# Kernel optimization log

Measured on AMD Instinct MI355X. Metric: run time of the kernel, lower is better.

Reference implementation:

```python
import jax, jax.numpy as jnp
import numpy as np

B = 65536
H = 1024          # hidden_dimension
D_OUT = 2         # output_dimension
N_EXPERTS = 10


def setup_inputs() -> dict:
    key = jax.random.key(0)
    ks = jax.random.split(key, 9)
    s = 0.02
    return {
        "x": jax.random.normal(ks[0], (B, 12), dtype=jnp.float32),
        "W1": jax.random.normal(ks[1], (H, 1), dtype=jnp.float32) * s,    # fc1 weight [out,in]
        "b1": jax.random.normal(ks[2], (H,), dtype=jnp.float32) * s,
        "Wmeta": jax.random.normal(ks[3], (N_EXPERTS, H), dtype=jnp.float32) * s,  # row i = fc_meta[i].weight[:,0]
        "bmeta": jax.random.normal(ks[4], (N_EXPERTS, H), dtype=jnp.float32) * s,  # row i = fc_meta[i].bias
        "W2": jax.random.normal(ks[5], (H, H), dtype=jnp.float32) * s,
        "b2": jax.random.normal(ks[6], (H,), dtype=jnp.float32) * s,
        "W3": jax.random.normal(ks[7], (D_OUT, H), dtype=jnp.float32) * s,
        "b3": jax.random.normal(ks[8], (D_OUT,), dtype=jnp.float32) * s,
    }


def reference(x, W1, b1, Wmeta, bmeta, W2, b2, W3, b3):
    one_hot = x[:, 0:10]          # [B, 10] expert selection weights
    delta = x[:, 10:11]           # [B, 1]
    phi = x[:, 11:12]             # [B, 1]
    # fc1(delta): [B,1] @ [1,H]
    x1 = delta * W1[:, 0] + b1    # [B, H]
    # expert i output: phi * Wmeta[i] + bmeta[i]; one-hot weighted sum over experts
    # sum_i one_hot[:,i]*(phi*Wmeta[i]+bmeta[i]) = phi*(one_hot@Wmeta) + one_hot@bmeta
    x2 = phi * (one_hot @ Wmeta) + one_hot @ bmeta  # [B, H]
    h = jax.nn.relu(x1 + x2)
    h = jax.nn.relu(h @ W2.T + b2)                  # fc2 + relu
    return h @ W3.T + b3                            # fc3 -> [B, 2]
```

## Files before the change

kernel.cpp:

```cpp
#include <hip/hip_runtime.h>
#include <stdint.h>

#define NROWS 65536
#define HD 1024

typedef __attribute__((ext_vector_type(8))) short bf16x8;
typedef __attribute__((ext_vector_type(16))) float f32x16;

typedef __attribute__((address_space(1))) const unsigned int* gas_ptr;
typedef __attribute__((address_space(3))) unsigned int* las_ptr;

__device__ __forceinline__ unsigned short f2bf(float f) {
  union { float f; uint32_t u; } v; v.f = f;
  uint32_t u = v.u;
  return (unsigned short)((u + 0x7fffu + ((u >> 16) & 1u)) >> 16);
}

__device__ __forceinline__ void gl16(const void* g, void* l) {
  __builtin_amdgcn_global_load_lds((gas_ptr)g, (las_ptr)l, 16, 0, 0);
}

__global__ void k_w2pk(const float* __restrict__ W2, unsigned short* __restrict__ W2pk) {
  int i = blockIdx.x * 256 + threadIdx.x;
  int lane = i & 63, f = (i >> 6) & 15, T = (i >> 10) & 15, ct = i >> 14;
  int kl = f & 1, p = (f >> 1) & 1, cb = (f >> 2) & 1, wn = f >> 3;
  int col = ct * 128 + wn * 64 + cb * 32 + (lane & 31);
  int k = T * 64 + p * 32 + kl * 16 + (lane >> 5) * 8;
  const float4* s4 = (const float4*)(W2 + (size_t)col * HD + k);
  float4 a = s4[0], b = s4[1];
  uint4 pk;
  pk.x = (uint32_t)f2bf(a.x) | ((uint32_t)f2bf(a.y) << 16);
  pk.y = (uint32_t)f2bf(a.z) | ((uint32_t)f2bf(a.w) << 16);
  pk.z = (uint32_t)f2bf(b.x) | ((uint32_t)f2bf(b.y) << 16);
  pk.w = (uint32_t)f2bf(b.z) | ((uint32_t)f2bf(b.w) << 16);
  *(uint4*)(W2pk + (size_t)i * 8) = pk;
}

__global__ __launch_bounds__(512) void k_layer1(
    const float* __restrict__ x, const float* __restrict__ W1,
    const float* __restrict__ b1, const float* __restrict__ Wmeta,
    const float* __restrict__ bmeta, unsigned short* __restrict__ h) {
  __shared__ float xs[64 * 12];
  int r0 = blockIdx.x * 64;
  int t = threadIdx.x;
  int j0 = t * 2;
  float w1a = W1[j0], w1b = W1[j0 + 1];
  float b1a = b1[j0], b1b = b1[j0 + 1];
  float wma[10], wmb[10], bma[10], bmb[10];
#pragma unroll
  for (int e = 0; e < 10; e++) {
    float2 wmv = *(const float2*)(Wmeta + e * HD + j0);
    float2 bmv = *(const float2*)(bmeta + e * HD + j0);
    wma[e] = wmv.x; wmb[e] = wmv.y; bma[e] = bmv.x; bmb[e] = bmv.y;
  }
  for (int i = t; i < 64 * 12; i += 512) xs[i] = x[(size_t)r0 * 12 + i];
  __syncthreads();
  int g = j0 >> 3;
  for (int r = 0; r < 64; r++) {
    const float* xr = xs + r * 12;
    float delta = xr[10], phi = xr[11];
    float s1a = 0.f, s1b = 0.f, s2a = 0.f, s2b = 0.f;
#pragma unroll
    for (int e = 0; e < 10; e++) {
      float oh = xr[e];
      s1a = fmaf(oh, wma[e], s1a);
      s1b = fmaf(oh, wmb[e], s1b);
      s2a = fmaf(oh, bma[e], s2a);
      s2b = fmaf(oh, bmb[e], s2b);
    }
    float pa = fmaf(delta, w1a, b1a) + fmaf(phi, s1a, s2a);
    float pb = fmaf(delta, w1b, b1b) + fmaf(phi, s1b, s2b);
    pa = fmaxf(pa, 0.f); pb = fmaxf(pb, 0.f);
    uint32_t pk = (uint32_t)f2bf(pa) | ((uint32_t)f2bf(pb) << 16);
    int rr = r0 + r;
    int gs = (g & 124) | ((g & 3) ^ ((rr >> 1) & 3));
    *(uint32_t*)(h + (size_t)rr * HD + gs * 8 + (j0 & 7)) = pk;
  }
}

__global__ __launch_bounds__(256, 4) void k_gemm(
    const unsigned short* __restrict__ h, const unsigned short* __restrict__ W2pk,
    const float* __restrict__ b2, const float* __restrict__ W3,
    float* __restrict__ partial) {
  __shared__ char lds[34816];
  int tid = threadIdx.x;
  int b = (int)blockIdx.x;
  int bx = ((b & 7) << 9) | (b >> 3);
  int rt = bx >> 3, ct = bx & 7;
  size_t r0 = (size_t)rt * 128;
  int c0 = ct * 128;
  int w = tid >> 6, lane = tid & 63;
  int wm = w >> 1, wn = w & 1;
  int l31 = lane & 31, hi = lane >> 5;
  int sw = (l31 >> 1) & 3;

  f32x16 acc[2][2];
#pragma unroll
  for (int rb = 0; rb < 2; rb++)
#pragma unroll
    for (int cb = 0; cb < 2; cb++)
#pragma unroll
      for (int i = 0; i < 16; i++) acc[rb][cb][i] = 0.f;

  int arow0 = (wm * 64 + 0  + l31) * 64;
  int arow1 = (wm * 64 + 32 + l31) * 64;
  const unsigned short* bwave = W2pk + ((size_t)ct * 16 * 16 + (size_t)wn * 8) * 512 + lane * 8;

  for (int T = 0; T < 16; T++) {
    const unsigned short* bt = bwave + (size_t)T * 16 * 512;
    bf16x8 B[2][4];
#pragma unroll
    for (int cb = 0; cb < 2; cb++)
#pragma unroll
      for (int pk = 0; pk < 4; pk++)
        B[cb][pk] = *(const bf16x8*)(bt + (cb * 4 + pk) * 512);
#pragma unroll
    for (int q = 0; q < 2; q++) {
      int s = tid + 256 * q;
      int row = s >> 2, g4 = s & 3;
      const unsigned short* hsrc = h + (r0 + row) * (size_t)HD + T * 64 + g4 * 8;
      gl16(hsrc,      lds +        (size_t)s * 16);
      gl16(hsrc + 32, lds + 8192 + (size_t)s * 16);
    }
    __syncthreads();
#pragma unroll
    for (int p = 0; p < 2; p++) {
      const char* lA = lds + p * 8192;
#pragma unroll
      for (int kl = 0; kl < 2; kl++) {
        int slot = ((kl * 2 + hi) ^ sw) << 4;
        bf16x8 a0 = *(const bf16x8*)(lA + arow0 + slot);
        bf16x8 a1 = *(const bf16x8*)(lA + arow1 + slot);
        acc[0][0] = __builtin_amdgcn_mfma_f32_32x32x16_bf16(a0, B[0][p * 2 + kl], acc[0][0], 0, 0, 0);
        acc[0][1] = __builtin_amdgcn_mfma_f32_32x32x16_bf16(a0, B[1][p * 2 + kl], acc[0][1], 0, 0, 0);
        acc[1][0] = __builtin_amdgcn_mfma_f32_32x32x16_bf16(a1, B[0][p * 2 + kl], acc[1][0], 0, 0, 0);
        acc[1][1] = __builtin_amdgcn_mfma_f32_32x32x16_bf16(a1, B[1][p * 2 + kl], acc[1][1], 0, 0, 0);
      }
    }
    __syncthreads();
  }

  float b2c[2], w30[2], w31[2];
#pragma unroll
  for (int cb = 0; cb < 2; cb++) {
    int c = c0 + wn * 64 + cb * 32 + l31;
    b2c[cb] = b2[c];
    w30[cb] = W3[c];
    w31[cb] = W3[HD + c];
  }
  float2* sE = (float2*)lds;
#pragma unroll
  for (int rb = 0; rb < 2; rb++) {
    __syncthreads();
#pragma unroll
    for (int reg = 0; reg < 16; reg++) {
      float v0 = fmaxf(acc[rb][0][reg] + b2c[0], 0.f);
      float v1 = fmaxf(acc[rb][1][reg] + b2c[1], 0.f);
      float2 o;
      o.x = v0 * w30[0] + v1 * w30[1];
      o.y = v0 * w31[0] + v1 * w31[1];
      int rowf = (reg & 3) + 8 * (reg >> 2) + 4 * hi;
      int line = (wm * 32 + rowf) * 2 + wn;
      sE[line * 33 + l31] = o;
    }
    __syncthreads();
    int half = tid & 1, tgt = tid >> 1;
    int d = tgt & 1, rowf_t = (tgt >> 1) & 31, bi = tgt >> 6;
    int line0 = (bi * 32 + rowf_t) * 2 + half;
    const float* sf = (const float*)lds;
    float s = 0.f;
#pragma unroll
    for (int j = 0; j < 32; j++) s += sf[(line0 * 33 + j) * 2 + d];
    s += __shfl_xor(s, 1);
    if (half == 0) {
      int row = bi * 64 + rb * 32 + rowf_t;
      partial[(size_t)ct * (NROWS * 2) + (r0 + row) * 2 + d] = s;
    }
  }
}

__global__ void k_reduce(const float* __restrict__ partial, const float* __restrict__ b3,
                         float* __restrict__ out) {
  int i = blockIdx.x * 256 + threadIdx.x;
  float s = b3[i & 1];
#pragma unroll
  for (int ctt = 0; ctt < 8; ctt++) s += partial[(size_t)ctt * 131072 + i];
  out[i] = s;
}

extern "C" void kernel_launch(void* const* d_in, const int* in_sizes, int n_in,
                              void* d_out, int out_size, void* d_ws, size_t ws_size,
                              hipStream_t stream) {
  const float* x     = (const float*)d_in[0];
  const float* W1    = (const float*)d_in[1];
  const float* b1    = (const float*)d_in[2];
  const float* Wmeta = (const float*)d_in[3];
  const float* bmeta = (const float*)d_in[4];
  const float* W2    = (const float*)d_in[5];
  const float* b2    = (const float*)d_in[6];
  const float* W3    = (const float*)d_in[7];
  const float* b3    = (const float*)d_in[8];
  float* out = (float*)d_out;

  char* ws = (char*)d_ws;
  unsigned short* hbuf  = (unsigned short*)ws;
  unsigned short* W2pk  = (unsigned short*)(ws + (size_t)NROWS * HD * 2);
  float* partial = (float*)(ws + (size_t)NROWS * HD * 2 + (size_t)HD * HD * 2);

  k_w2pk<<<512, 256, 0, stream>>>(W2, W2pk);
  k_layer1<<<1024, 512, 0, stream>>>(x, W1, b1, Wmeta, bmeta, hbuf);
  k_gemm<<<4096, 256, 0, stream>>>(hbuf, W2pk, b2, W3, partial);
  k_reduce<<<512, 256, 0, stream>>>(partial, b3, out);
}
```

Measured before the change: 204.6 us.

## Restructure fc2 GEMM into per-wave 64x64 tiles with double-buffered A/B prefetch

```diff
diff --git a/kernel.cpp b/kernel.cpp
--- a/kernel.cpp
+++ b/kernel.cpp
@@ -22,9 +22,9 @@
 
 __global__ void k_w2pk(const float* __restrict__ W2, unsigned short* __restrict__ W2pk) {
   int i = blockIdx.x * 256 + threadIdx.x;
-  int lane = i & 63, f = (i >> 6) & 15, T = (i >> 10) & 15, ct = i >> 14;
-  int kl = f & 1, p = (f >> 1) & 1, cb = (f >> 2) & 1, wn = f >> 3;
-  int col = ct * 128 + wn * 64 + cb * 32 + (lane & 31);
+  int lane = i & 63, f = (i >> 6) & 7, T = (i >> 9) & 15, ct = i >> 13;
+  int kl = f & 1, p = (f >> 1) & 1, cb = f >> 2;
+  int col = ct * 64 + cb * 32 + (lane & 31);
   int k = T * 64 + p * 32 + kl * 16 + (lane >> 5) * 8;
   const float4* s4 = (const float4*)(W2 + (size_t)col * HD + k);
   float4 a = s4[0], b = s4[1];
@@ -73,26 +73,25 @@
     pa = fmaxf(pa, 0.f); pb = fmaxf(pb, 0.f);
     uint32_t pk = (uint32_t)f2bf(pa) | ((uint32_t)f2bf(pb) << 16);
     int rr = r0 + r;
-    int gs = (g & 124) | ((g & 3) ^ ((rr >> 1) & 3));
+    int gs = (g & 120) | ((g & 7) ^ (rr & 7));
     *(uint32_t*)(h + (size_t)rr * HD + gs * 8 + (j0 & 7)) = pk;
   }
 }
 
-__global__ __launch_bounds__(256, 4) void k_gemm(
+__global__ __launch_bounds__(256, 2) void k_gemm(
     const unsigned short* __restrict__ h, const unsigned short* __restrict__ W2pk,
     const float* __restrict__ b2, const float* __restrict__ W3,
     float* __restrict__ partial) {
-  __shared__ char lds[34816];
+  __shared__ char lds[65536];
   int tid = threadIdx.x;
   int b = (int)blockIdx.x;
   int bx = ((b & 7) << 9) | (b >> 3);
-  int rt = bx >> 3, ct = bx & 7;
-  size_t r0 = (size_t)rt * 128;
-  int c0 = ct * 128;
+  int rblk = bx >> 4, ct = bx & 15;
+  size_t r0 = (size_t)rblk * 256;
+  int c0 = ct * 64;
   int w = tid >> 6, lane = tid & 63;
-  int wm = w >> 1, wn = w & 1;
   int l31 = lane & 31, hi = lane >> 5;
-  int sw = (l31 >> 1) & 3;
+  char* ldsw = lds + w * 16384;
 
   f32x16 acc[2][2];
 #pragma unroll
@@ -102,79 +101,81 @@
 #pragma unroll
       for (int i = 0; i < 16; i++) acc[rb][cb][i] = 0.f;
 
-  int arow0 = (wm * 64 + 0  + l31) * 64;
-  int arow1 = (wm * 64 + 32 + l31) * 64;
-  const unsigned short* bwave = W2pk + ((size_t)ct * 16 * 16 + (size_t)wn * 8) * 512 + lane * 8;
-
+  const unsigned short* aSrc = h + (r0 + w * 64 + (lane >> 3)) * (size_t)HD + (lane & 7) * 8;
+  const unsigned short* bSrc = W2pk + ((size_t)ct * 8192 + lane) * 8;
+
+#define STAGE_A(T, BUF)                                                           \
+  do {                                                                            \
+    _Pragma("unroll")                                                             \
+    for (int q = 0; q < 8; q++)                                                   \
+      gl16(aSrc + (size_t)q * 8 * HD + (T) * 64,                                  \
+           ldsw + (BUF) * 8192 + q * 1024 + (lane & 63) * 16);                    \
+  } while (0)
+
+  bf16x8 B[2][8];
+  STAGE_A(0, 0);
+#pragma unroll
+  for (int f = 0; f < 8; f++) B[0][f] = *(const bf16x8*)(bSrc + (0 * 512 + f * 64) * 8);
+
+  int slotBase = l31 & 7;
+#pragma unroll
   for (int T = 0; T < 16; T++) {
-    const unsigned short* bt = bwave + (size_t)T * 16 * 512;
-    bf16x8 B[2][4];
-#pragma unroll
-    for (int cb = 0; cb < 2; cb++)
-#pragma unroll
-      for (int pk = 0; pk < 4; pk++)
-        B[cb][pk] = *(const bf16x8*)(bt + (cb * 4 + pk) * 512);
-#pragma unroll
-    for (int q = 0; q < 2; q++) {
-      int s = tid + 256 * q;
-      int row = s >> 2, g4 = s & 3;
-      const unsigned short* hsrc = h + (r0 + row) * (size_t)HD + T * 64 + g4 * 8;
-      gl16(hsrc,      lds +        (size_t)s * 16);
-      gl16(hsrc + 32, lds + 8192 + (size_t)s * 16);
-    }
-    __syncthreads();
-#pragma unroll
-    for (int p = 0; p < 2; p++) {
-      const char* lA = lds + p * 8192;
-#pragma unroll
-      for (int kl = 0; kl < 2; kl++) {
-        int slot = ((kl * 2 + hi) ^ sw) << 4;
-        bf16x8 a0 = *(const bf16x8*)(lA + arow0 + slot);
-        bf16x8 a1 = *(const bf16x8*)(lA + arow1 + slot);
-        acc[0][0] = __builtin_amdgcn_mfma_f32_32x32x16_bf16(a0, B[0][p * 2 + kl], acc[0][0], 0, 0, 0);
-        acc[0][1] = __builtin_amdgcn_mfma_f32_32x32x16_bf16(a0, B[1][p * 2 + kl], acc[0][1], 0, 0, 0);
-        acc[1][0] = __builtin_amdgcn_mfma_f32_32x32x16_bf16(a1, B[0][p * 2 + kl], acc[1][0], 0, 0, 0);
-        acc[1][1] = __builtin_amdgcn_mfma_f32_32x32x16_bf16(a1, B[1][p * 2 + kl], acc[1][1], 0, 0, 0);
-      }
-    }
-    __syncthreads();
+    const int cur = T & 1, nxt = cur ^ 1;
+    if (T < 15) {
+      STAGE_A(T + 1, nxt);
+#pragma unroll
+      for (int f = 0; f < 8; f++)
+        B[nxt][f] = *(const bf16x8*)(bSrc + ((T + 1) * 512 + f * 64) * 8);
+    }
+    if (T < 15) { asm volatile("s_waitcnt vmcnt(16)" ::: "memory"); }
+    else        { asm volatile("s_waitcnt vmcnt(0)" ::: "memory"); }
+    __builtin_amdgcn_sched_barrier(0);
+    bf16x8 a0[4], a1[4];
+#pragma unroll
+    for (int s = 0; s < 4; s++) {
+      int sl = ((s * 2 + hi) ^ slotBase) << 4;
+      a0[s] = *(const bf16x8*)(ldsw + cur * 8192 + l31 * 128 + sl);
+      a1[s] = *(const bf16x8*)(ldsw + cur * 8192 + (l31 + 32) * 128 + sl);
+    }
+    asm volatile("s_waitcnt lgkmcnt(0)" ::: "memory");
+    __builtin_amdgcn_sched_barrier(0);
+    __builtin_amdgcn_s_setprio(1);
+#pragma unroll
+    for (int s = 0; s < 4; s++) {
+      acc[0][0] = __builtin_amdgcn_mfma_f32_32x32x16_bf16(a0[s], B[cur][s],     acc[0][0], 0, 0, 0);
+      acc[0][1] = __builtin_amdgcn_mfma_f32_32x32x16_bf16(a0[s], B[cur][4 + s], acc[0][1], 0, 0, 0);
+      acc[1][0] = __builtin_amdgcn_mfma_f32_32x32x16_bf16(a1[s], B[cur][s],     acc[1][0], 0, 0, 0);
+      acc[1][1] = __builtin_amdgcn_mfma_f32_32x32x16_bf16(a1[s], B[cur][4 + s], acc[1][1], 0, 0, 0);
+    }
+    __builtin_amdgcn_s_setprio(0);
   }
 
   float b2c[2], w30[2], w31[2];
 #pragma unroll
   for (int cb = 0; cb < 2; cb++) {
-    int c = c0 + wn * 64 + cb * 32 + l31;
+    int c = c0 + cb * 32 + l31;
     b2c[cb] = b2[c];
     w30[cb] = W3[c];
     w31[cb] = W3[HD + c];
   }
-  float2* sE = (float2*)lds;
 #pragma unroll
   for (int rb = 0; rb < 2; rb++) {
-    __syncthreads();
 #pragma unroll
     for (int reg = 0; reg < 16; reg++) {
       float v0 = fmaxf(acc[rb][0][reg] + b2c[0], 0.f);
       float v1 = fmaxf(acc[rb][1][reg] + b2c[1], 0.f);
-      float2 o;
-      o.x = v0 * w30[0] + v1 * w30[1];
-      o.y = v0 * w31[0] + v1 * w31[1];
-      int rowf = (reg & 3) + 8 * (reg >> 2) + 4 * hi;
-      int line = (wm * 32 + rowf) * 2 + wn;
-      sE[line * 33 + l31] = o;
-    }
-    __syncthreads();
-    int half = tid & 1, tgt = tid >> 1;
-    int d = tgt & 1, rowf_t = (tgt >> 1) & 31, bi = tgt >> 6;
-    int line0 = (bi * 32 + rowf_t) * 2 + half;
-    const float* sf = (const float*)lds;
-    float s = 0.f;
-#pragma unroll
-    for (int j = 0; j < 32; j++) s += sf[(line0 * 33 + j) * 2 + d];
-    s += __shfl_xor(s, 1);
-    if (half == 0) {
-      int row = bi * 64 + rb * 32 + rowf_t;
-      partial[(size_t)ct * (NROWS * 2) + (r0 + row) * 2 + d] = s;
+      float o0 = fmaf(v0, w30[0], v1 * w30[1]);
+      float o1 = fmaf(v0, w31[0], v1 * w31[1]);
+#pragma unroll
+      for (int m = 16; m >= 1; m >>= 1) {
+        o0 += __shfl_xor(o0, m);
+        o1 += __shfl_xor(o1, m);
+      }
+      if (l31 == 0) {
+        size_t row = r0 + w * 64 + rb * 32 + (reg & 3) + 8 * (reg >> 2) + 4 * hi;
+        float2 o; o.x = o0; o.y = o1;
+        *(float2*)(partial + (size_t)ct * (NROWS * 2) + row * 2) = o;
+      }
     }
   }
 }
@@ -184,7 +185,7 @@
   int i = blockIdx.x * 256 + threadIdx.x;
   float s = b3[i & 1];
 #pragma unroll
-  for (int ctt = 0; ctt < 8; ctt++) s += partial[(size_t)ctt * 131072 + i];
+  for (int ctt = 0; ctt < 16; ctt++) s += partial[(size_t)ctt * 131072 + i];
   out[i] = s;
 }
 
```

New measurement: 267.5 us. +30.7%, slower.

## Triple-buffer A tiles and double-buffer B fragments in GEMM; merge prep kernels

Applied to the files above, without the earlier changes.

```diff
diff --git a/kernel.cpp b/kernel.cpp
--- a/kernel.cpp
+++ b/kernel.cpp
@@ -20,28 +20,29 @@
   __builtin_amdgcn_global_load_lds((gas_ptr)g, (las_ptr)l, 16, 0, 0);
 }
 
-__global__ void k_w2pk(const float* __restrict__ W2, unsigned short* __restrict__ W2pk) {
-  int i = blockIdx.x * 256 + threadIdx.x;
-  int lane = i & 63, f = (i >> 6) & 15, T = (i >> 10) & 15, ct = i >> 14;
-  int kl = f & 1, p = (f >> 1) & 1, cb = (f >> 2) & 1, wn = f >> 3;
-  int col = ct * 128 + wn * 64 + cb * 32 + (lane & 31);
-  int k = T * 64 + p * 32 + kl * 16 + (lane >> 5) * 8;
-  const float4* s4 = (const float4*)(W2 + (size_t)col * HD + k);
-  float4 a = s4[0], b = s4[1];
-  uint4 pk;
-  pk.x = (uint32_t)f2bf(a.x) | ((uint32_t)f2bf(a.y) << 16);
-  pk.y = (uint32_t)f2bf(a.z) | ((uint32_t)f2bf(a.w) << 16);
-  pk.z = (uint32_t)f2bf(b.x) | ((uint32_t)f2bf(b.y) << 16);
-  pk.w = (uint32_t)f2bf(b.z) | ((uint32_t)f2bf(b.w) << 16);
-  *(uint4*)(W2pk + (size_t)i * 8) = pk;
-}
-
-__global__ __launch_bounds__(512) void k_layer1(
+__global__ __launch_bounds__(512) void k_prep(
     const float* __restrict__ x, const float* __restrict__ W1,
     const float* __restrict__ b1, const float* __restrict__ Wmeta,
-    const float* __restrict__ bmeta, unsigned short* __restrict__ h) {
+    const float* __restrict__ bmeta, const float* __restrict__ W2,
+    unsigned short* __restrict__ h, unsigned short* __restrict__ W2pk) {
   __shared__ float xs[64 * 12];
-  int r0 = blockIdx.x * 64;
+  if (blockIdx.x < 256) {
+    int i = blockIdx.x * 512 + threadIdx.x;
+    int lane = i & 63, f = (i >> 6) & 15, T = (i >> 10) & 15, ct = i >> 14;
+    int kl = f & 1, p = (f >> 1) & 1, cb = (f >> 2) & 1, wn = f >> 3;
+    int col = ct * 128 + wn * 64 + cb * 32 + (lane & 31);
+    int k = T * 64 + p * 32 + kl * 16 + (lane >> 5) * 8;
+    const float4* s4 = (const float4*)(W2 + (size_t)col * HD + k);
+    float4 a = s4[0], b = s4[1];
+    uint4 pk;
+    pk.x = (uint32_t)f2bf(a.x) | ((uint32_t)f2bf(a.y) << 16);
+    pk.y = (uint32_t)f2bf(a.z) | ((uint32_t)f2bf(a.w) << 16);
+    pk.z = (uint32_t)f2bf(b.x) | ((uint32_t)f2bf(b.y) << 16);
+    pk.w = (uint32_t)f2bf(b.z) | ((uint32_t)f2bf(b.w) << 16);
+    *(uint4*)(W2pk + (size_t)i * 8) = pk;
+    return;
+  }
+  int r0 = ((int)blockIdx.x - 256) * 64;
   int t = threadIdx.x;
   int j0 = t * 2;
   float w1a = W1[j0], w1b = W1[j0 + 1];
@@ -78,11 +79,11 @@
   }
 }
 
-__global__ __launch_bounds__(256, 4) void k_gemm(
+__global__ __launch_bounds__(256, 3) void k_gemm(
     const unsigned short* __restrict__ h, const unsigned short* __restrict__ W2pk,
     const float* __restrict__ b2, const float* __restrict__ W3,
     float* __restrict__ partial) {
-  __shared__ char lds[34816];
+  __shared__ char lds[49152];
   int tid = threadIdx.x;
   int b = (int)blockIdx.x;
   int bx = ((b & 7) << 9) | (b >> 3);
@@ -93,6 +94,8 @@
   int wm = w >> 1, wn = w & 1;
   int l31 = lane & 31, hi = lane >> 5;
   int sw = (l31 >> 1) & 3;
+  int s0 = (hi ^ sw) << 4;
+  int s1 = ((2 + hi) ^ sw) << 4;
 
   f32x16 acc[2][2];
 #pragma unroll
@@ -104,41 +107,93 @@
 
   int arow0 = (wm * 64 + 0  + l31) * 64;
   int arow1 = (wm * 64 + 32 + l31) * 64;
-  const unsigned short* bwave = W2pk + ((size_t)ct * 16 * 16 + (size_t)wn * 8) * 512 + lane * 8;
-
-  for (int T = 0; T < 16; T++) {
-    const unsigned short* bt = bwave + (size_t)T * 16 * 512;
-    bf16x8 B[2][4];
-#pragma unroll
-    for (int cb = 0; cb < 2; cb++)
-#pragma unroll
-      for (int pk = 0; pk < 4; pk++)
-        B[cb][pk] = *(const bf16x8*)(bt + (cb * 4 + pk) * 512);
-#pragma unroll
-    for (int q = 0; q < 2; q++) {
-      int s = tid + 256 * q;
-      int row = s >> 2, g4 = s & 3;
-      const unsigned short* hsrc = h + (r0 + row) * (size_t)HD + T * 64 + g4 * 8;
-      gl16(hsrc,      lds +        (size_t)s * 16);
-      gl16(hsrc + 32, lds + 8192 + (size_t)s * 16);
-    }
-    __syncthreads();
-#pragma unroll
-    for (int p = 0; p < 2; p++) {
-      const char* lA = lds + p * 8192;
-#pragma unroll
-      for (int kl = 0; kl < 2; kl++) {
-        int slot = ((kl * 2 + hi) ^ sw) << 4;
-        bf16x8 a0 = *(const bf16x8*)(lA + arow0 + slot);
-        bf16x8 a1 = *(const bf16x8*)(lA + arow1 + slot);
-        acc[0][0] = __builtin_amdgcn_mfma_f32_32x32x16_bf16(a0, B[0][p * 2 + kl], acc[0][0], 0, 0, 0);
-        acc[0][1] = __builtin_amdgcn_mfma_f32_32x32x16_bf16(a0, B[1][p * 2 + kl], acc[0][1], 0, 0, 0);
-        acc[1][0] = __builtin_amdgcn_mfma_f32_32x32x16_bf16(a1, B[0][p * 2 + kl], acc[1][0], 0, 0, 0);
-        acc[1][1] = __builtin_amdgcn_mfma_f32_32x32x16_bf16(a1, B[1][p * 2 + kl], acc[1][1], 0, 0, 0);
-      }
-    }
-    __syncthreads();
-  }
+  const unsigned short* bwave = W2pk + ((size_t)ct * 256 + (size_t)wn * 8) * 512 + lane * 8;
+
+#define STAGE_A(T, SB)                                                            \
+  do {                                                                            \
+    _Pragma("unroll")                                                             \
+    for (int q = 0; q < 2; q++) {                                                 \
+      int s = tid + 256 * q;                                                      \
+      int row = s >> 2, g4 = s & 3;                                               \
+      const unsigned short* hsrc = h + (r0 + row) * (size_t)HD + (T) * 64 + g4 * 8; \
+      gl16(hsrc,      lds + (SB) +        (size_t)s * 16);                        \
+      gl16(hsrc + 32, lds + (SB) + 8192 + (size_t)s * 16);                        \
+    }                                                                             \
+  } while (0)
+
+#define GBODY(T, BC, BN)                                                          \
+  do {                                                                            \
+    const char* lA0 = lds + slotT;                                                \
+    const char* lA1 = lds + slotT + 8192;                                         \
+    bf16x8 a00 = *(const bf16x8*)(lA0 + arow0 + s0);              \
+    bf16x8 a01 = *(const bf16x8*)(lA0 + arow1 + s0);                              \
+    bf16x8 a02 = *(const bf16x8*)(lA0 + arow0 + s1);                  \
+    bf16x8 a03 = *(const bf16x8*)(lA0 + arow1 + s1);                              \
+    bf16x8 a10 = *(const bf16x8*)(lA1 + arow0 + s0);                  \
+    bf16x8 a11 = *(const bf16x8*)(lA1 + arow1 + s0);                              \
+    bf16x8 a12 = *(const bf16x8*)(lA1 + arow0 + s1);                  \
+    bf16x8 a13 = *(const bf16x8*)(lA1 + arow1 + s1);                              \
+    if ((T) < 14) STAGE_A((T) + 2, slotS);                                        \
+    const unsigned short* btn = bwave + (size_t)((T) + 1) * 8192;                 \
+    if ((T) < 15) {                                                               \
+      BN[0] = *(const bf16x8*)(btn + 0 * 512);                                    \
+      BN[1] = *(const bf16x8*)(btn + 1 * 512);                                    \
+      BN[2] = *(const bf16x8*)(btn + 2 * 512);                                    \
+      BN[3] = *(const bf16x8*)(btn + 3 * 512);                                    \
+    }                                                                             \
+    if ((T) <= 13)      { asm volatile("s_waitcnt vmcnt(8)" ::: "memory"); }      \
+    else if ((T) == 14) { asm volatile("s_waitcnt vmcnt(4)" ::: "memory"); }      \
+    else                { asm volatile("s_waitcnt vmcnt(0)" ::: "memory"); }      \
+    asm volatile("s_waitcnt lgkmcnt(0)" ::: "memory");                            \
+    __builtin_amdgcn_sched_barrier(0);                                            \
+    __builtin_amdgcn_s_setprio(1);                                                \
+    acc[0][0] = __builtin_amdgcn_mfma_f32_32x32x16_bf16(a00, BC[0], acc[0][0], 0, 0, 0); \
+    acc[1][0] = __builtin_amdgcn_mfma_f32_32x32x16_bf16(a01, BC[0], acc[1][0], 0, 0, 0); \
+    acc[0][0] = __builtin_amdgcn_mfma_f32_32x32x16_bf16(a02, BC[1], acc[0][0], 0, 0, 0); \
+    acc[1][0] = __builtin_amdgcn_mfma_f32_32x32x16_bf16(a03, BC[1], acc[1][0], 0, 0, 0); \
+    acc[0][0] = __builtin_amdgcn_mfma_f32_32x32x16_bf16(a10, BC[2], acc[0][0], 0, 0, 0); \
+    acc[1][0] = __builtin_amdgcn_mfma_f32_32x32x16_bf16(a11, BC[2], acc[1][0], 0, 0, 0); \
+    acc[0][0] = __builtin_amdgcn_mfma_f32_32x32x16_bf16(a12, BC[3], acc[0][0], 0, 0, 0); \
+    acc[1][0] = __builtin_amdgcn_mfma_f32_32x32x16_bf16(a13, BC[3], acc[1][0], 0, 0, 0); \
+    __builtin_amdgcn_s_setprio(0);                                                \
+    if ((T) < 15) {                                                               \
+      BN[4] = *(const bf16x8*)(btn + 4 * 512);                                    \
+      BN[5] = *(const bf16x8*)(btn + 5 * 512);                                    \
+      BN[6] = *(const bf16x8*)(btn + 6 * 512);                                    \
+      BN[7] = *(const bf16x8*)(btn + 7 * 512);                                    \
+    }                                                                             \
+    __builtin_amdgcn_s_setprio(1);                                                \
+    acc[0][1] = __builtin_amdgcn_mfma_f32_32x32x16_bf16(a00, BC[4], acc[0][1], 0, 0, 0); \
+    acc[1][1] = __builtin_amdgcn_mfma_f32_32x32x16_bf16(a01, BC[4], acc[1][1], 0, 0, 0); \
+    acc[0][1] = __builtin_amdgcn_mfma_f32_32x32x16_bf16(a02, BC[5], acc[0][1], 0, 0, 0); \
+    acc[1][1] = __builtin_amdgcn_mfma_f32_32x32x16_bf16(a03, BC[5], acc[1][1], 0, 0, 0); \
+    acc[0][1] = __builtin_amdgcn_mfma_f32_32x32x16_bf16(a10, BC[6], acc[0][1], 0, 0, 0); \
+    acc[1][1] = __builtin_amdgcn_mfma_f32_32x32x16_bf16(a11, BC[6], acc[1][1], 0, 0, 0); \
+    acc[0][1] = __builtin_amdgcn_mfma_f32_32x32x16_bf16(a12, BC[7], acc[0][1], 0, 0, 0); \
+    acc[1][1] = __builtin_amdgcn_mfma_f32_32x32x16_bf16(a13, BC[7], acc[1][1], 0, 0, 0); \
+    __builtin_amdgcn_s_setprio(0);                                                \
+    __builtin_amdgcn_s_barrier();                                                 \
+    slotT += 16384; if (slotT == 49152) slotT = 0;                                \
+    slotS += 16384; if (slotS == 49152) slotS = 0;                                \
+  } while (0)
+
+  bf16x8 B0s[8], B1s[8];
+  {
+    const unsigned short* bt0 = bwave;
+#pragma unroll
+    for (int f = 0; f < 8; f++) B0s[f] = *(const bf16x8*)(bt0 + f * 512);
+  }
+  STAGE_A(0, 0);
+  STAGE_A(1, 16384);
+  asm volatile("s_waitcnt vmcnt(4)" ::: "memory");
+  __builtin_amdgcn_s_barrier();
+
+  int slotT = 0, slotS = 32768;
+  for (int TT = 0; TT < 8; TT++) {
+    GBODY(TT * 2,     B0s, B1s);
+    GBODY(TT * 2 + 1, B1s, B0s);
+  }
+  __syncthreads();
 
   float b2c[2], w30[2], w31[2];
 #pragma unroll
@@ -207,8 +262,7 @@
   unsigned short* W2pk  = (unsigned short*)(ws + (size_t)NROWS * HD * 2);
   float* partial = (float*)(ws + (size_t)NROWS * HD * 2 + (size_t)HD * HD * 2);
 
-  k_w2pk<<<512, 256, 0, stream>>>(W2, W2pk);
-  k_layer1<<<1024, 512, 0, stream>>>(x, W1, b1, Wmeta, bmeta, hbuf);
+  k_prep<<<1280, 512, 0, stream>>>(x, W1, b1, Wmeta, bmeta, W2, hbuf, W2pk);
   k_gemm<<<4096, 256, 0, stream>>>(hbuf, W2pk, b2, W3, partial);
   k_reduce<<<512, 256, 0, stream>>>(partial, b3, out);
 }
```

New measurement: 214.5 us. 1.05x slower.

## Fuse prep kernels and replace partial-sum reduce with shuffle reduction plus atomics

Applied to the files above, without the earlier changes.

```diff
diff --git a/kernel.cpp b/kernel.cpp
--- a/kernel.cpp
+++ b/kernel.cpp
@@ -20,28 +20,31 @@
   __builtin_amdgcn_global_load_lds((gas_ptr)g, (las_ptr)l, 16, 0, 0);
 }
 
-__global__ void k_w2pk(const float* __restrict__ W2, unsigned short* __restrict__ W2pk) {
-  int i = blockIdx.x * 256 + threadIdx.x;
-  int lane = i & 63, f = (i >> 6) & 15, T = (i >> 10) & 15, ct = i >> 14;
-  int kl = f & 1, p = (f >> 1) & 1, cb = (f >> 2) & 1, wn = f >> 3;
-  int col = ct * 128 + wn * 64 + cb * 32 + (lane & 31);
-  int k = T * 64 + p * 32 + kl * 16 + (lane >> 5) * 8;
-  const float4* s4 = (const float4*)(W2 + (size_t)col * HD + k);
-  float4 a = s4[0], b = s4[1];
-  uint4 pk;
-  pk.x = (uint32_t)f2bf(a.x) | ((uint32_t)f2bf(a.y) << 16);
-  pk.y = (uint32_t)f2bf(a.z) | ((uint32_t)f2bf(a.w) << 16);
-  pk.z = (uint32_t)f2bf(b.x) | ((uint32_t)f2bf(b.y) << 16);
-  pk.w = (uint32_t)f2bf(b.z) | ((uint32_t)f2bf(b.w) << 16);
-  *(uint4*)(W2pk + (size_t)i * 8) = pk;
-}
-
-__global__ __launch_bounds__(512) void k_layer1(
+__global__ __launch_bounds__(512) void k_prep(
     const float* __restrict__ x, const float* __restrict__ W1,
     const float* __restrict__ b1, const float* __restrict__ Wmeta,
-    const float* __restrict__ bmeta, unsigned short* __restrict__ h) {
+    const float* __restrict__ bmeta, const float* __restrict__ W2,
+    const float* __restrict__ b3, unsigned short* __restrict__ h,
+    unsigned short* __restrict__ W2pk, float* __restrict__ out) {
   __shared__ float xs[64 * 12];
-  int r0 = blockIdx.x * 64;
+  if (blockIdx.x < 256) {
+    int i = blockIdx.x * 512 + threadIdx.x;
+    out[i] = b3[i & 1];
+    int lane = i & 63, f = (i >> 6) & 15, T = (i >> 10) & 15, ct = i >> 14;
+    int kl = f & 1, p = (f >> 1) & 1, cb = (f >> 2) & 1, wn = f >> 3;
+    int col = ct * 128 + wn * 64 + cb * 32 + (lane & 31);
+    int k = T * 64 + p * 32 + kl * 16 + (lane >> 5) * 8;
+    const float4* s4 = (const float4*)(W2 + (size_t)col * HD + k);
+    float4 a = s4[0], b = s4[1];
+    uint4 pk;
+    pk.x = (uint32_t)f2bf(a.x) | ((uint32_t)f2bf(a.y) << 16);
+    pk.y = (uint32_t)f2bf(a.z) | ((uint32_t)f2bf(a.w) << 16);
+    pk.z = (uint32_t)f2bf(b.x) | ((uint32_t)f2bf(b.y) << 16);
+    pk.w = (uint32_t)f2bf(b.z) | ((uint32_t)f2bf(b.w) << 16);
+    *(uint4*)(W2pk + (size_t)i * 8) = pk;
+    return;
+  }
+  int r0 = ((int)blockIdx.x - 256) * 64;
   int t = threadIdx.x;
   int j0 = t * 2;
   float w1a = W1[j0], w1b = W1[j0 + 1];
@@ -81,8 +84,8 @@
 __global__ __launch_bounds__(256, 4) void k_gemm(
     const unsigned short* __restrict__ h, const unsigned short* __restrict__ W2pk,
     const float* __restrict__ b2, const float* __restrict__ W3,
-    float* __restrict__ partial) {
-  __shared__ char lds[34816];
+    float* __restrict__ out) {
+  __shared__ char lds[16384];
   int tid = threadIdx.x;
   int b = (int)blockIdx.x;
   int bx = ((b & 7) << 9) | (b >> 3);
@@ -148,44 +151,26 @@
     w30[cb] = W3[c];
     w31[cb] = W3[HD + c];
   }
-  float2* sE = (float2*)lds;
 #pragma unroll
   for (int rb = 0; rb < 2; rb++) {
-    __syncthreads();
 #pragma unroll
     for (int reg = 0; reg < 16; reg++) {
       float v0 = fmaxf(acc[rb][0][reg] + b2c[0], 0.f);
       float v1 = fmaxf(acc[rb][1][reg] + b2c[1], 0.f);
-      float2 o;
-      o.x = v0 * w30[0] + v1 * w30[1];
-      o.y = v0 * w31[0] + v1 * w31[1];
-      int rowf = (reg & 3) + 8 * (reg >> 2) + 4 * hi;
-      int line = (wm * 32 + rowf) * 2 + wn;
-      sE[line * 33 + l31] = o;
-    }
-    __syncthreads();
-    int half = tid & 1, tgt = tid >> 1;
-    int d = tgt & 1, rowf_t = (tgt >> 1) & 31, bi = tgt >> 6;
-    int line0 = (bi * 32 + rowf_t) * 2 + half;
-    const float* sf = (const float*)lds;
-    float s = 0.f;
+      float o0 = fmaf(v0, w30[0], v1 * w30[1]);
+      float o1 = fmaf(v0, w31[0], v1 * w31[1]);
 #pragma unroll
-    for (int j = 0; j < 32; j++) s += sf[(line0 * 33 + j) * 2 + d];
-    s += __shfl_xor(s, 1);
-    if (half == 0) {
-      int row = bi * 64 + rb * 32 + rowf_t;
-      partial[(size_t)ct * (NROWS * 2) + (r0 + row) * 2 + d] = s;
+      for (int m = 1; m <= 16; m <<= 1) {
+        o0 += __shfl_xor(o0, m);
+        o1 += __shfl_xor(o1, m);
+      }
+      if (l31 == 0) {
+        size_t row = r0 + wm * 64 + rb * 32 + (reg & 3) + 8 * (reg >> 2) + 4 * hi;
+        atomicAdd(&out[row * 2 + 0], o0);
+        atomicAdd(&out[row * 2 + 1], o1);
+      }
     }
   }
-}
-
-__global__ void k_reduce(const float* __restrict__ partial, const float* __restrict__ b3,
-                         float* __restrict__ out) {
-  int i = blockIdx.x * 256 + threadIdx.x;
-  float s = b3[i & 1];
-#pragma unroll
-  for (int ctt = 0; ctt < 8; ctt++) s += partial[(size_t)ctt * 131072 + i];
-  out[i] = s;
 }
 
 extern "C" void kernel_launch(void* const* d_in, const int* in_sizes, int n_in,
@@ -205,10 +190,7 @@
   char* ws = (char*)d_ws;
   unsigned short* hbuf  = (unsigned short*)ws;
   unsigned short* W2pk  = (unsigned short*)(ws + (size_t)NROWS * HD * 2);
-  float* partial = (float*)(ws + (size_t)NROWS * HD * 2 + (size_t)HD * HD * 2);
 
-  k_w2pk<<<512, 256, 0, stream>>>(W2, W2pk);
-  k_layer1<<<1024, 512, 0, stream>>>(x, W1, b1, Wmeta, bmeta, hbuf);
-  k_gemm<<<4096, 256, 0, stream>>>(hbuf, W2pk, b2, W3, partial);
-  k_reduce<<<512, 256, 0, stream>>>(partial, b3, out);
+  k_prep<<<1280, 512, 0, stream>>>(x, W1, b1, Wmeta, bmeta, W2, b3, hbuf, W2pk, out);
+  k_gemm<<<4096, 256, 0, stream>>>(hbuf, W2pk, b2, W3, out);
 }
```

After: 255.3 us. 1.25x slower.
